# Optimization experiments

Measured on AMD Instinct MI355X. Metric: run time of the kernel, lower is better.

## Reference

```python
import jax, jax.numpy as jnp
import numpy as np

B = 1
E = 8388608                      # embedding size (dim 1)
NNZ = 131072                     # inhibition links
MIN_SPARSITY = 0.002
MAX_SPARSITY = 0.02
BOOST_PERCENT = 1e-8             # forward default boost_percent
MAX_ACTIVE = int(np.ceil(MAX_SPARSITY * E))    # 167773, torch uses .item() -> static
MIN_ACTIVE = int(np.floor(MIN_SPARSITY * E))   # 16777


def setup_inputs() -> dict:
    key = jax.random.key(0)
    k1, k3, k4, k5 = jax.random.split(key, 4)
    x = jax.random.normal(k1, (B, E, 1, 1), dtype=jnp.float32)
    boost_tensor = jnp.zeros((B, E, 1, 1), dtype=jnp.float32)   # initial boost state (zeros_like in module)
    inh_affector = jax.random.randint(k3, (NNZ,), 0, E, dtype=jnp.int32)
    inh_affectee = jax.random.randint(k4, (NNZ,), 0, E, dtype=jnp.int32)
    # inhibition values are negative (self-inhibition, affect_value=-0.01 scale)
    inh_values = -jax.random.uniform(k5, (NNZ,), dtype=jnp.float32) * 0.05
    return {"x": x, "boost_tensor": boost_tensor, "inh_values": inh_values,
            "inh_affector": inh_affector, "inh_affectee": inh_affectee}


def reference(x, boost_tensor, inh_values, inh_affector, inh_affectee):
    xf = x.reshape(B, E)
    bf = boost_tensor.reshape(B, E)

    # --- run_boosting: PercentClosenessBoosting (units far from max get boosted) ---
    boost_new = bf + (1.0 - xf / jnp.max(xf)) * jnp.float32(BOOST_PERCENT)
    boosted = jnp.maximum(xf, 0.0) + boost_new   # tensor_above + boost_tensor

    # --- apply_sparse_self_affector: tens[affectee] += tens[affector] * values ---
    # RHS gathered from the pre-update tensor, scatter-add onto affectee coords.
    inhibited = boosted.at[0, inh_affectee].add(boosted[0, inh_affector] * inh_values)

    # --- run_k_winners_positive: keep top max_active per row, binarize positives ---
    topv, topi = jax.lax.top_k(inhibited, MAX_ACTIVE)          # [B, K]
    rows = jnp.arange(B)[:, None]
    result = jnp.zeros((B, E), dtype=jnp.float32).at[rows, topi].set(
        (topv > 0).astype(jnp.float32))

    # --- choose_boosted_to_satisfy_minimum ---
    actually_active = jnp.sum(result)
    _, boost_idx = jax.lax.top_k(boost_new, MIN_ACTIVE)        # [B, MIN_ACTIVE]
    to_activate = jnp.ceil(jnp.float32(MIN_ACTIVE) - actually_active)
    need = actually_active < jnp.float32(MIN_ACTIVE)
    add = need & (jnp.arange(MIN_ACTIVE, dtype=jnp.float32) < to_activate)
    add = jnp.broadcast_to(add.astype(jnp.float32), (B, MIN_ACTIVE))
    out = result.at[rows, boost_idx].max(add)

    return out.reshape(B, E, 1, 1)
```

## Files before the change

### kernel.cpp

```cpp
#include <hip/hip_runtime.h>
#include <stdint.h>

#define E_SIZE   8388608
#define N4       (E_SIZE / 4)
#define NNZ_SZ   131072
#define K_ACT    167773
#define MIN_ACT  16777
#define CAP      262144
#define BCAP     2048
#define TINY_F   9.5367431640625e-7f
#define NBINS    16384
#define SHIFT1   18

__device__ __forceinline__ unsigned int f2A(float f) {
    unsigned int u = __float_as_uint(f);
    return (u & 0x80000000u) ? ~u : (u | 0x80000000u);
}
__device__ __forceinline__ unsigned int f2D(float f) { return ~f2A(f); }
__device__ __forceinline__ float A2f(unsigned int A) {
    unsigned int u = (A & 0x80000000u) ? (A & 0x7FFFFFFFu) : ~A;
    return __uint_as_float(u);
}
__device__ __forceinline__ float D2f(unsigned int D) { return A2f(~D); }

__device__ __forceinline__ float boostedf(float v, float b, float mx) {
    return fmaxf(v, 0.0f) + (b + (1.0f - v / mx) * 1e-8f);
}
__device__ __forceinline__ unsigned int binclamp14(float v) {
    return (v < TINY_F) ? (NBINS - 1u) : (f2D(v) >> SHIFT1);
}


__device__ void block_select(const unsigned int* counts, int nbins, unsigned int Krem,
                             unsigned int* res, unsigned int* scratch) {
    int t = threadIdx.x;
    int per = nbins >> 10; if (per == 0) per = 1;
    int nth = nbins / per;
    unsigned int part = 0;
    if (t < nth)
        for (int j = 0; j < per; j++) part += counts[t * per + j];
    scratch[t] = part;
    unsigned int ws = part;
    for (int off = 32; off; off >>= 1) ws += __shfl_down(ws, off, 64);
    if ((t & 63) == 0) scratch[1024 + (t >> 6)] = ws;
    __syncthreads();
    if (t == 0) {
        unsigned int cum = 0;
        int w = 0;
        for (; w < 15; w++) {
            unsigned int s = scratch[1024 + w];
            if (cum + s >= Krem) break;
            cum += s;
        }
        int tt = w * 64, te = tt + 63;
        for (; tt < te; tt++) {
            unsigned int s = scratch[tt];
            if (cum + s >= Krem) break;
            cum += s;
        }
        int b = tt * per, be = b + per - 1;
        for (; b < be; b++) {
            unsigned int s = counts[b];
            if (cum + s >= Krem) break;
            cum += s;
        }
        res[0] = (unsigned int)b;
        res[1] = Krem - cum;
    }
    __syncthreads();
}

__global__ void __launch_bounds__(256)
k_max(const float4* __restrict__ x, unsigned int* __restrict__ pmax,
      unsigned int* __restrict__ ctrl, unsigned int* __restrict__ hist) {
    int t = threadIdx.x, blk = blockIdx.x;
    if (blk == 0 && t < 64) ctrl[t] = 0u;
    if (t < 16) hist[blk * 16 + t] = 0u;
    int tid = blk * 256 + t;
    unsigned int m = 0u;
    for (int i = tid; i < N4; i += 1024 * 256) {
        float4 v = x[i];
        m = max(m, f2A(v.x)); m = max(m, f2A(v.y));
        m = max(m, f2A(v.z)); m = max(m, f2A(v.w));
    }
    for (int off = 32; off; off >>= 1)
        m = max(m, __shfl_down(m, off, 64));
    __shared__ unsigned int sm[4];
    if ((t & 63) == 0) sm[t >> 6] = m;
    __syncthreads();
    if (t == 0) pmax[blk] = max(max(sm[0], sm[1]), max(sm[2], sm[3]));
}

__device__ __forceinline__ float reduce_pmax(const unsigned int* __restrict__ pmax,
                                             unsigned int* smax) {
    int t = threadIdx.x;
    unsigned int m = pmax[t];
    for (int off = 32; off; off >>= 1)
        m = max(m, __shfl_down(m, off, 64));
    if ((t & 63) == 0) smax[t >> 6] = m;
    __syncthreads();
    if (t == 0) {
        unsigned int r = smax[0];
        for (int i = 1; i < 16; i++) r = max(r, smax[i]);
        smax[0] = r;
    }
    __syncthreads();
    return A2f(smax[0]);
}

__global__ void __launch_bounds__(1024)
k_boost_hist(const float4* __restrict__ x, const float4* __restrict__ bf,
             float4* __restrict__ out, const unsigned int* __restrict__ pmax,
             unsigned int* __restrict__ hist) {
    __shared__ unsigned int h[NBINS];
    __shared__ unsigned int smax[16];
    float mx = reduce_pmax(pmax, smax);
    int t = threadIdx.x;
    for (int i = t; i < NBINS; i += 1024) h[i] = 0u;
    __syncthreads();
    unsigned int tiny = 0;
    int gtid = blockIdx.x * 1024 + t;
    for (int i = gtid; i < N4; i += 256 * 1024) {
        float4 v = x[i], b = bf[i];
        float4 r;
        r.x = boostedf(v.x, b.x, mx);
        r.y = boostedf(v.y, b.y, mx);
        r.z = boostedf(v.z, b.z, mx);
        r.w = boostedf(v.w, b.w, mx);
        out[i] = r;
        #define HISTONE(c) { if ((c) < TINY_F) tiny++; \
            else atomicAdd(&h[f2D(c) >> SHIFT1], 1u); }
        HISTONE(r.x); HISTONE(r.y); HISTONE(r.z); HISTONE(r.w);
        #undef HISTONE
    }
    for (int off = 32; off; off >>= 1)
        tiny += __shfl_down(tiny, off, 64);
    if ((t & 63) == 0 && tiny) atomicAdd(&h[NBINS - 1], tiny);
    __syncthreads();
    for (int k = t; k < NBINS; k += 1024) {
        unsigned int c = h[k];
        if (c) atomicAdd(&hist[k], c);
    }
}

__global__ void __launch_bounds__(1024)
k_scatter(const float* __restrict__ x, const float* __restrict__ bf,
          const float* __restrict__ vals, const int* __restrict__ aff,
          const int* __restrict__ afe, float* __restrict__ inh,
          const unsigned int* __restrict__ pmax, unsigned int* __restrict__ hist) {
    __shared__ int shi[NBINS];
    __shared__ unsigned int smax[16];
    float mx = reduce_pmax(pmax, smax);
    int t = threadIdx.x;
    for (int i = t; i < NBINS; i += 1024) shi[i] = 0;
    __syncthreads();
    int i = blockIdx.x * 1024 + t;
    int a = aff[i], e = afe[i];
    float bo = boostedf(x[a], bf[a], mx);
    float contrib = bo * vals[i];
    float old = atomicAdd(&inh[e], contrib);
    float nw = old + contrib;
    unsigned int ob = binclamp14(old), nb = binclamp14(nw);
    if (ob != nb) {
        atomicAdd(&shi[nb], 1);
        atomicAdd(&shi[ob], -1);
    }
    __syncthreads();
    for (int k = t; k < NBINS; k += 1024) {
        int v = shi[k];
        if (v) atomicAdd((int*)&hist[k], v);
    }
}

__global__ void __launch_bounds__(1024)
k_scan1(const unsigned int* __restrict__ hist, unsigned int* __restrict__ ctrl) {
    __shared__ unsigned int scratch[1040];
    __shared__ unsigned int res[2];
    block_select(hist, NBINS, (unsigned int)K_ACT, res, scratch);
    if (threadIdx.x == 0) { ctrl[1] = res[0]; ctrl[2] = res[1]; }
}

__global__ void __launch_bounds__(1024)
k_markcompact(float4* __restrict__ out, const unsigned int* __restrict__ ctrl,
              unsigned int* __restrict__ ctrlw, unsigned int* __restrict__ gidx,
              unsigned int* __restrict__ gD) {
    __shared__ unsigned int cidx[BCAP];
    __shared__ unsigned int cDs[BCAP];
    __shared__ unsigned int scnt, sbase;
    int t = threadIdx.x;
    if (t == 0) scnt = 0;
    __syncthreads();
    unsigned int b1 = ctrl[1];
    int gtid = blockIdx.x * 1024 + t;
    for (int i = gtid; i < N4; i += 256 * 1024) {
        float4 f = out[i];
        float4 r;
        #define MARKONE(c, rr, comp) { \
            unsigned int bc = binclamp14(c); \
            if (bc < b1) rr = ((c) > 0.0f) ? 1.0f : 0.0f; \
            else { rr = 0.0f; if (bc == b1) { \
                unsigned int p = atomicAdd(&scnt, 1u); \
                if (p < BCAP) { cidx[p] = (unsigned int)i * 4u + comp; cDs[p] = f2D(c); } } } }
        MARKONE(f.x, r.x, 0u); MARKONE(f.y, r.y, 1u);
        MARKONE(f.z, r.z, 2u); MARKONE(f.w, r.w, 3u);
        #undef MARKONE
        out[i] = r;
    }
    __syncthreads();
    if (t == 0) {
        unsigned int m = min(scnt, (unsigned int)BCAP);
        scnt = m;
        sbase = atomicAdd(&ctrlw[7], m);
    }
    __syncthreads();
    unsigned int m = scnt, base = sbase;
    for (unsigned int i = t; i < m; i += 1024) {
        unsigned int g = base + i;
        if (g < CAP) { gidx[g] = cidx[i]; gD[g] = cDs[i]; }
    }
}

__global__ void __launch_bounds__(1024)
k_select(float* __restrict__ out, const unsigned int* __restrict__ ctrl,
         const unsigned int* __restrict__ gidx, const unsigned int* __restrict__ gD) {
    __shared__ unsigned int h512[512];
    __shared__ unsigned int scratch[1040];
    __shared__ unsigned int res[2];
    __shared__ unsigned int ties[128];
    __shared__ unsigned int tcnt;
    int t = threadIdx.x;
    unsigned int nc = min(ctrl[7], (unsigned int)CAP);
    unsigned int Krem = ctrl[2];
    unsigned int b1 = ctrl[1];

    if (t < 512) h512[t] = 0u;
    if (t == 0) tcnt = 0u;
    __syncthreads();
    for (unsigned int i = t; i < nc; i += 1024)
        atomicAdd(&h512[(gD[i] >> 9) & 511u], 1u);
    __syncthreads();
    block_select(h512, 512, Krem, res, scratch);
    unsigned int b2 = res[0], Krem2 = res[1];

    if (t < 512) h512[t] = 0u;
    __syncthreads();
    for (unsigned int i = t; i < nc; i += 1024) {
        unsigned int D = gD[i];
        if (((D >> 9) & 511u) == b2) atomicAdd(&h512[D & 511u], 1u);
    }
    __syncthreads();
    block_select(h512, 512, Krem2, res, scratch);
    unsigned int b3 = res[0], need = res[1];
    unsigned int T = (b1 << SHIFT1) | (b2 << 9) | b3;

    for (unsigned int i = t; i < nc; i += 1024) {
        if (gD[i] == T) {
            unsigned int p = atomicAdd(&tcnt, 1u);
            if (p < 128) ties[p] = gidx[i];
        }
    }
    __syncthreads();
    unsigned int M = min(tcnt, 128u);
    float val = (D2f(T) > 0.0f) ? 1.0f : 0.0f;
    for (unsigned int i = t; i < M; i += 1024) {
        unsigned int idx = ties[i];
        unsigned int rank = 0;
        for (unsigned int j = 0; j < M; j++) rank += (ties[j] < idx) ? 1u : 0u;
        if (rank < need) out[idx] = val;
    }
    for (unsigned int i = t; i < nc; i += 1024) {
        unsigned int D = gD[i];
        if (D < T) out[gidx[i]] = (D2f(D) > 0.0f) ? 1.0f : 0.0f;
    }
}

extern "C" void kernel_launch(void* const* d_in, const int* in_sizes, int n_in,
                              void* d_out, int out_size, void* d_ws, size_t ws_size,
                              hipStream_t stream) {
    const float* x    = (const float*)d_in[0];
    const float* bf   = (const float*)d_in[1];
    const float* vals = (const float*)d_in[2];
    const int*   aff  = (const int*)d_in[3];
    const int*   afe  = (const int*)d_in[4];
    float* out = (float*)d_out;

    unsigned int* ctrl = (unsigned int*)d_ws;
    unsigned int* pmax = (unsigned int*)((char*)d_ws + 4096);
    unsigned int* hist = (unsigned int*)((char*)d_ws + 8192);
    unsigned int* gidx = (unsigned int*)((char*)d_ws + 8192 + (size_t)NBINS * 4);
    unsigned int* gD   = (unsigned int*)((char*)d_ws + 8192 + (size_t)NBINS * 4 + (size_t)CAP * 4);

    k_max<<<1024, 256, 0, stream>>>((const float4*)x, pmax, ctrl, hist);
    k_boost_hist<<<256, 1024, 0, stream>>>((const float4*)x, (const float4*)bf,
                                           (float4*)out, pmax, hist);
    k_scatter<<<NNZ_SZ / 1024, 1024, 0, stream>>>(x, bf, vals, aff, afe, out, pmax, hist);
    k_scan1<<<1, 1024, 0, stream>>>(hist, ctrl);
    k_markcompact<<<256, 1024, 0, stream>>>((float4*)out, ctrl, ctrl, gidx, gD);
    k_select<<<1, 1024, 0, stream>>>(out, ctrl, gidx, gD);
}
```

Measured before the change: 187.7 us.

## Fuse all six stages into one cooperative kernel with grid syncs

Replaces the six separate launches with one cooperative kernel of 256 blocks, using grid.sync between the max, boost/histogram, scatter, scan, mark/compact and final select phases. This removes the per-launch overhead and the gaps between launches, and lets each block run the bin-select scan on the histogram itself instead of a separate single-block kernel. The scatter phase now does its histogram-correction atomics straight to global memory rather than through a shared histogram. In exchange it adds the cost of grid-wide barriers and needs all 256 blocks of 1024 threads, each holding about 90KB of shared memory, to be resident at the same time. Blocks other than block 0 sit idle during the final select phase.

```diff
diff --git a/kernel.cpp b/kernel.cpp
--- a/kernel.cpp
+++ b/kernel.cpp
@@ -1,5 +1,8 @@
 #include <hip/hip_runtime.h>
+#include <hip/hip_cooperative_groups.h>
 #include <stdint.h>
+
+namespace cg = cooperative_groups;
 
 #define E_SIZE   8388608
 #define N4       (E_SIZE / 4)
@@ -11,6 +14,8 @@
 #define TINY_F   9.5367431640625e-7f
 #define NBINS    16384
 #define SHIFT1   18
+#define NBLK     256
+#define NTHR     1024
 
 __device__ __forceinline__ unsigned int f2A(float f) {
     unsigned int u = __float_as_uint(f);
@@ -29,7 +34,6 @@
 __device__ __forceinline__ unsigned int binclamp14(float v) {
     return (v < TINY_F) ? (NBINS - 1u) : (f2D(v) >> SHIFT1);
 }
-
 
 __device__ void block_select(const unsigned int* counts, int nbins, unsigned int Krem,
                              unsigned int* res, unsigned int* scratch) {
@@ -70,130 +74,110 @@
     __syncthreads();
 }
 
-__global__ void __launch_bounds__(256)
-k_max(const float4* __restrict__ x, unsigned int* __restrict__ pmax,
-      unsigned int* __restrict__ ctrl, unsigned int* __restrict__ hist) {
-    int t = threadIdx.x, blk = blockIdx.x;
+__global__ void __launch_bounds__(NTHR, 4)
+k_fused(const float* __restrict__ x, const float* __restrict__ bf,
+        const float* __restrict__ vals, const int* __restrict__ aff,
+        const int* __restrict__ afe, float* __restrict__ out,
+        unsigned int* __restrict__ ctrl, unsigned int* __restrict__ pmax,
+        unsigned int* __restrict__ hist, unsigned int* __restrict__ gidx,
+        unsigned int* __restrict__ gD) {
+    cg::grid_group grid = cg::this_grid();
+    __shared__ unsigned int h[NBINS];
+    __shared__ unsigned int scratch[1040];
+    __shared__ unsigned int res[2];
+    __shared__ unsigned int smax[16];
+    __shared__ unsigned int cidx[BCAP];
+    __shared__ unsigned int cDs[BCAP];
+    __shared__ unsigned int ties[128];
+    __shared__ unsigned int scnt, sbase, tcnt;
+
+    const int t = threadIdx.x;
+    const int blk = blockIdx.x;
+    const float4* __restrict__ x4 = (const float4*)x;
+    const float4* __restrict__ bf4 = (const float4*)bf;
+    float4* __restrict__ out4 = (float4*)out;
+
     if (blk == 0 && t < 64) ctrl[t] = 0u;
-    if (t < 16) hist[blk * 16 + t] = 0u;
-    int tid = blk * 256 + t;
-    unsigned int m = 0u;
-    for (int i = tid; i < N4; i += 1024 * 256) {
-        float4 v = x[i];
-        m = max(m, f2A(v.x)); m = max(m, f2A(v.y));
-        m = max(m, f2A(v.z)); m = max(m, f2A(v.w));
-    }
-    for (int off = 32; off; off >>= 1)
-        m = max(m, __shfl_down(m, off, 64));
-    __shared__ unsigned int sm[4];
-    if ((t & 63) == 0) sm[t >> 6] = m;
-    __syncthreads();
-    if (t == 0) pmax[blk] = max(max(sm[0], sm[1]), max(sm[2], sm[3]));
-}
-
-__device__ __forceinline__ float reduce_pmax(const unsigned int* __restrict__ pmax,
-                                             unsigned int* smax) {
-    int t = threadIdx.x;
-    unsigned int m = pmax[t];
-    for (int off = 32; off; off >>= 1)
-        m = max(m, __shfl_down(m, off, 64));
-    if ((t & 63) == 0) smax[t >> 6] = m;
-    __syncthreads();
-    if (t == 0) {
-        unsigned int r = smax[0];
-        for (int i = 1; i < 16; i++) r = max(r, smax[i]);
-        smax[0] = r;
-    }
-    __syncthreads();
-    return A2f(smax[0]);
-}
-
-__global__ void __launch_bounds__(1024)
-k_boost_hist(const float4* __restrict__ x, const float4* __restrict__ bf,
-             float4* __restrict__ out, const unsigned int* __restrict__ pmax,
-             unsigned int* __restrict__ hist) {
-    __shared__ unsigned int h[NBINS];
-    __shared__ unsigned int smax[16];
-    float mx = reduce_pmax(pmax, smax);
-    int t = threadIdx.x;
-    for (int i = t; i < NBINS; i += 1024) h[i] = 0u;
-    __syncthreads();
-    unsigned int tiny = 0;
-    int gtid = blockIdx.x * 1024 + t;
-    for (int i = gtid; i < N4; i += 256 * 1024) {
-        float4 v = x[i], b = bf[i];
-        float4 r;
-        r.x = boostedf(v.x, b.x, mx);
-        r.y = boostedf(v.y, b.y, mx);
-        r.z = boostedf(v.z, b.z, mx);
-        r.w = boostedf(v.w, b.w, mx);
-        out[i] = r;
-        #define HISTONE(c) { if ((c) < TINY_F) tiny++; \
-            else atomicAdd(&h[f2D(c) >> SHIFT1], 1u); }
-        HISTONE(r.x); HISTONE(r.y); HISTONE(r.z); HISTONE(r.w);
-        #undef HISTONE
-    }
-    for (int off = 32; off; off >>= 1)
-        tiny += __shfl_down(tiny, off, 64);
-    if ((t & 63) == 0 && tiny) atomicAdd(&h[NBINS - 1], tiny);
-    __syncthreads();
-    for (int k = t; k < NBINS; k += 1024) {
+    if (t < (NBINS / NBLK)) hist[blk * (NBINS / NBLK) + t] = 0u;
+    {
+        unsigned int m = 0u;
+        for (int i = blk * NTHR + t; i < N4; i += NBLK * NTHR) {
+            float4 v = x4[i];
+            m = max(m, f2A(v.x)); m = max(m, f2A(v.y));
+            m = max(m, f2A(v.z)); m = max(m, f2A(v.w));
+        }
+        for (int off = 32; off; off >>= 1) m = max(m, __shfl_down(m, off, 64));
+        if ((t & 63) == 0) smax[t >> 6] = m;
+        __syncthreads();
+        if (t == 0) {
+            unsigned int r = smax[0];
+            for (int i = 1; i < 16; i++) r = max(r, smax[i]);
+            pmax[blk] = r;
+        }
+    }
+    __threadfence();
+    grid.sync();
+
+    float mx;
+    {
+        unsigned int m = (t < NBLK) ? pmax[t] : 0u;
+        for (int off = 32; off; off >>= 1) m = max(m, __shfl_down(m, off, 64));
+        if (t < NBLK && (t & 63) == 0) smax[t >> 6] = m;
+        __syncthreads();
+        if (t == 0) smax[0] = max(max(smax[0], smax[1]), max(smax[2], smax[3]));
+        __syncthreads();
+        mx = A2f(smax[0]);
+    }
+    for (int i = t; i < NBINS; i += NTHR) h[i] = 0u;
+    __syncthreads();
+    {
+        unsigned int tiny = 0;
+        for (int i = blk * NTHR + t; i < N4; i += NBLK * NTHR) {
+            float4 v = x4[i], b = bf4[i];
+            float4 r;
+            r.x = boostedf(v.x, b.x, mx);
+            r.y = boostedf(v.y, b.y, mx);
+            r.z = boostedf(v.z, b.z, mx);
+            r.w = boostedf(v.w, b.w, mx);
+            out4[i] = r;
+            #define HISTONE(c) { if ((c) < TINY_F) tiny++; \
+                else atomicAdd(&h[f2D(c) >> SHIFT1], 1u); }
+            HISTONE(r.x); HISTONE(r.y); HISTONE(r.z); HISTONE(r.w);
+            #undef HISTONE
+        }
+        for (int off = 32; off; off >>= 1) tiny += __shfl_down(tiny, off, 64);
+        if ((t & 63) == 0 && tiny) atomicAdd(&h[NBINS - 1], tiny);
+    }
+    __syncthreads();
+    for (int k = t; k < NBINS; k += NTHR) {
         unsigned int c = h[k];
         if (c) atomicAdd(&hist[k], c);
     }
-}
-
-__global__ void __launch_bounds__(1024)
-k_scatter(const float* __restrict__ x, const float* __restrict__ bf,
-          const float* __restrict__ vals, const int* __restrict__ aff,
-          const int* __restrict__ afe, float* __restrict__ inh,
-          const unsigned int* __restrict__ pmax, unsigned int* __restrict__ hist) {
-    __shared__ int shi[NBINS];
-    __shared__ unsigned int smax[16];
-    float mx = reduce_pmax(pmax, smax);
-    int t = threadIdx.x;
-    for (int i = t; i < NBINS; i += 1024) shi[i] = 0;
-    __syncthreads();
-    int i = blockIdx.x * 1024 + t;
-    int a = aff[i], e = afe[i];
-    float bo = boostedf(x[a], bf[a], mx);
-    float contrib = bo * vals[i];
-    float old = atomicAdd(&inh[e], contrib);
-    float nw = old + contrib;
-    unsigned int ob = binclamp14(old), nb = binclamp14(nw);
-    if (ob != nb) {
-        atomicAdd(&shi[nb], 1);
-        atomicAdd(&shi[ob], -1);
-    }
-    __syncthreads();
-    for (int k = t; k < NBINS; k += 1024) {
-        int v = shi[k];
-        if (v) atomicAdd((int*)&hist[k], v);
-    }
-}
-
-__global__ void __launch_bounds__(1024)
-k_scan1(const unsigned int* __restrict__ hist, unsigned int* __restrict__ ctrl) {
-    __shared__ unsigned int scratch[1040];
-    __shared__ unsigned int res[2];
+    __threadfence();
+    grid.sync();
+
+    if (t < 512) {
+        int i = blk * 512 + t;
+        int a = aff[i], e = afe[i];
+        float bo = boostedf(x[a], bf[a], mx);
+        float contrib = bo * vals[i];
+        float old = atomicAdd(&out[e], contrib);
+        float nw = old + contrib;
+        unsigned int ob = binclamp14(old), nb = binclamp14(nw);
+        if (ob != nb) {
+            atomicAdd(&hist[nb], 1u);
+            atomicAdd((int*)&hist[ob], -1);
+        }
+    }
+    __threadfence();
+    grid.sync();
+
     block_select(hist, NBINS, (unsigned int)K_ACT, res, scratch);
-    if (threadIdx.x == 0) { ctrl[1] = res[0]; ctrl[2] = res[1]; }
-}
-
-__global__ void __launch_bounds__(1024)
-k_markcompact(float4* __restrict__ out, const unsigned int* __restrict__ ctrl,
-              unsigned int* __restrict__ ctrlw, unsigned int* __restrict__ gidx,
-              unsigned int* __restrict__ gD) {
-    __shared__ unsigned int cidx[BCAP];
-    __shared__ unsigned int cDs[BCAP];
-    __shared__ unsigned int scnt, sbase;
-    int t = threadIdx.x;
-    if (t == 0) scnt = 0;
-    __syncthreads();
-    unsigned int b1 = ctrl[1];
-    int gtid = blockIdx.x * 1024 + t;
-    for (int i = gtid; i < N4; i += 256 * 1024) {
-        float4 f = out[i];
+    unsigned int b1 = res[0], Krem = res[1];
+    if (t == 0) scnt = 0u;
+    __syncthreads();
+    for (int i = blk * NTHR + t; i < N4; i += NBLK * NTHR) {
+        float4 f = out4[i];
         float4 r;
         #define MARKONE(c, rr, comp) { \
             unsigned int bc = binclamp14(c); \
@@ -204,73 +188,68 @@
         MARKONE(f.x, r.x, 0u); MARKONE(f.y, r.y, 1u);
         MARKONE(f.z, r.z, 2u); MARKONE(f.w, r.w, 3u);
         #undef MARKONE
-        out[i] = r;
+        out4[i] = r;
     }
     __syncthreads();
     if (t == 0) {
-        unsigned int m = min(scnt, (unsigned int)BCAP);
-        scnt = m;
-        sbase = atomicAdd(&ctrlw[7], m);
-    }
-    __syncthreads();
-    unsigned int m = scnt, base = sbase;
-    for (unsigned int i = t; i < m; i += 1024) {
-        unsigned int g = base + i;
-        if (g < CAP) { gidx[g] = cidx[i]; gD[g] = cDs[i]; }
-    }
-}
-
-__global__ void __launch_bounds__(1024)
-k_select(float* __restrict__ out, const unsigned int* __restrict__ ctrl,
-         const unsigned int* __restrict__ gidx, const unsigned int* __restrict__ gD) {
-    __shared__ unsigned int h512[512];
-    __shared__ unsigned int scratch[1040];
-    __shared__ unsigned int res[2];
-    __shared__ unsigned int ties[128];
-    __shared__ unsigned int tcnt;
-    int t = threadIdx.x;
-    unsigned int nc = min(ctrl[7], (unsigned int)CAP);
-    unsigned int Krem = ctrl[2];
-    unsigned int b1 = ctrl[1];
-
-    if (t < 512) h512[t] = 0u;
-    if (t == 0) tcnt = 0u;
-    __syncthreads();
-    for (unsigned int i = t; i < nc; i += 1024)
-        atomicAdd(&h512[(gD[i] >> 9) & 511u], 1u);
-    __syncthreads();
-    block_select(h512, 512, Krem, res, scratch);
-    unsigned int b2 = res[0], Krem2 = res[1];
-
-    if (t < 512) h512[t] = 0u;
-    __syncthreads();
-    for (unsigned int i = t; i < nc; i += 1024) {
-        unsigned int D = gD[i];
-        if (((D >> 9) & 511u) == b2) atomicAdd(&h512[D & 511u], 1u);
-    }
-    __syncthreads();
-    block_select(h512, 512, Krem2, res, scratch);
-    unsigned int b3 = res[0], need = res[1];
-    unsigned int T = (b1 << SHIFT1) | (b2 << 9) | b3;
-
-    for (unsigned int i = t; i < nc; i += 1024) {
-        if (gD[i] == T) {
-            unsigned int p = atomicAdd(&tcnt, 1u);
-            if (p < 128) ties[p] = gidx[i];
-        }
-    }
-    __syncthreads();
-    unsigned int M = min(tcnt, 128u);
-    float val = (D2f(T) > 0.0f) ? 1.0f : 0.0f;
-    for (unsigned int i = t; i < M; i += 1024) {
-        unsigned int idx = ties[i];
-        unsigned int rank = 0;
-        for (unsigned int j = 0; j < M; j++) rank += (ties[j] < idx) ? 1u : 0u;
-        if (rank < need) out[idx] = val;
-    }
-    for (unsigned int i = t; i < nc; i += 1024) {
-        unsigned int D = gD[i];
-        if (D < T) out[gidx[i]] = (D2f(D) > 0.0f) ? 1.0f : 0.0f;
+        unsigned int m2 = min(scnt, (unsigned int)BCAP);
+        scnt = m2;
+        sbase = atomicAdd(&ctrl[7], m2);
+    }
+    __syncthreads();
+    {
+        unsigned int m2 = scnt, base = sbase;
+        for (unsigned int i = t; i < m2; i += NTHR) {
+            unsigned int g = base + i;
+            if (g < CAP) { gidx[g] = cidx[i]; gD[g] = cDs[i]; }
+        }
+    }
+    __threadfence();
+    grid.sync();
+
+    if (blk != 0) return;
+    {
+        unsigned int nc = min(ctrl[7], (unsigned int)CAP);
+
+        if (t < 512) h[t] = 0u;
+        if (t == 0) tcnt = 0u;
+        __syncthreads();
+        for (unsigned int i = t; i < nc; i += NTHR)
+            atomicAdd(&h[(gD[i] >> 9) & 511u], 1u);
+        __syncthreads();
+        block_select(h, 512, Krem, res, scratch);
+        unsigned int b2 = res[0], Krem2 = res[1];
+
+        if (t < 512) h[t] = 0u;
+        __syncthreads();
+        for (unsigned int i = t; i < nc; i += NTHR) {
+            unsigned int D = gD[i];
+            if (((D >> 9) & 511u) == b2) atomicAdd(&h[D & 511u], 1u);
+        }
+        __syncthreads();
+        block_select(h, 512, Krem2, res, scratch);
+        unsigned int b3 = res[0], need = res[1];
+        unsigned int T = (b1 << SHIFT1) | (b2 << 9) | b3;
+
+        for (unsigned int i = t; i < nc; i += NTHR) {
+            if (gD[i] == T) {
+                unsigned int p = atomicAdd(&tcnt, 1u);
+                if (p < 128) ties[p] = gidx[i];
+            }
+        }
+        __syncthreads();
+        unsigned int M = min(tcnt, 128u);
+        float val = (D2f(T) > 0.0f) ? 1.0f : 0.0f;
+        for (unsigned int i = t; i < M; i += NTHR) {
+            unsigned int idx = ties[i];
+            unsigned int rank = 0;
+            for (unsigned int j = 0; j < M; j++) rank += (ties[j] < idx) ? 1u : 0u;
+            if (rank < need) out[idx] = val;
+        }
+        for (unsigned int i = t; i < nc; i += NTHR) {
+            unsigned int D = gD[i];
+            if (D < T) out[gidx[i]] = (D2f(D) > 0.0f) ? 1.0f : 0.0f;
+        }
     }
 }
 
@@ -290,11 +269,8 @@
     unsigned int* gidx = (unsigned int*)((char*)d_ws + 8192 + (size_t)NBINS * 4);
     unsigned int* gD   = (unsigned int*)((char*)d_ws + 8192 + (size_t)NBINS * 4 + (size_t)CAP * 4);
 
-    k_max<<<1024, 256, 0, stream>>>((const float4*)x, pmax, ctrl, hist);
-    k_boost_hist<<<256, 1024, 0, stream>>>((const float4*)x, (const float4*)bf,
-                                           (float4*)out, pmax, hist);
-    k_scatter<<<NNZ_SZ / 1024, 1024, 0, stream>>>(x, bf, vals, aff, afe, out, pmax, hist);
-    k_scan1<<<1, 1024, 0, stream>>>(hist, ctrl);
-    k_markcompact<<<256, 1024, 0, stream>>>((float4*)out, ctrl, ctrl, gidx, gD);
-    k_select<<<1, 1024, 0, stream>>>(out, ctrl, gidx, gD);
-}
+    void* args[] = { &x, &bf, &vals, &aff, &afe, &out,
+                     &ctrl, &pmax, &hist, &gidx, &gD };
+    hipLaunchCooperativeKernel((void*)k_fused, dim3(NBLK), dim3(NTHR),
+                               args, 0, stream);
+}
```

Result: slower. 586.7 us (+212.5%).

## Fuse threshold scan into mark-compact, drop shared histogram in scatter, double grids

Applied to the files above, without the earlier changes.

The single-block histogram scan kernel is folded into the mark/compact kernel: every block now redoes the 16384-bin select itself, and block 0 publishes the threshold bin and remaining count to new control slots. This removes one serial launch. The scatter kernel stops zeroing and flushing a 16384-entry shared histogram and updates the global histogram atomically only when a bin changes. Grid sizes for the boost/histogram and mark kernels go from 256 to 512 blocks. The trade-off is redundant scan work in each block and more global atomics in scatter. The change also relies on ctrl[32]/ctrl[33] being valid workspace slots.

```diff
diff --git a/kernel.cpp b/kernel.cpp
--- a/kernel.cpp
+++ b/kernel.cpp
@@ -29,7 +29,6 @@
 __device__ __forceinline__ unsigned int binclamp14(float v) {
     return (v < TINY_F) ? (NBINS - 1u) : (f2D(v) >> SHIFT1);
 }
-
 
 __device__ void block_select(const unsigned int* counts, int nbins, unsigned int Krem,
                              unsigned int* res, unsigned int* scratch) {
@@ -120,7 +119,7 @@
     __syncthreads();
     unsigned int tiny = 0;
     int gtid = blockIdx.x * 1024 + t;
-    for (int i = gtid; i < N4; i += 256 * 1024) {
+    for (int i = gtid; i < N4; i += 512 * 1024) {
         float4 v = x[i], b = bf[i];
         float4 r;
         r.x = boostedf(v.x, b.x, mx);
@@ -148,13 +147,9 @@
           const float* __restrict__ vals, const int* __restrict__ aff,
           const int* __restrict__ afe, float* __restrict__ inh,
           const unsigned int* __restrict__ pmax, unsigned int* __restrict__ hist) {
-    __shared__ int shi[NBINS];
     __shared__ unsigned int smax[16];
     float mx = reduce_pmax(pmax, smax);
-    int t = threadIdx.x;
-    for (int i = t; i < NBINS; i += 1024) shi[i] = 0;
-    __syncthreads();
-    int i = blockIdx.x * 1024 + t;
+    int i = blockIdx.x * 1024 + threadIdx.x;
     int a = aff[i], e = afe[i];
     float bo = boostedf(x[a], bf[a], mx);
     float contrib = bo * vals[i];
@@ -162,37 +157,33 @@
     float nw = old + contrib;
     unsigned int ob = binclamp14(old), nb = binclamp14(nw);
     if (ob != nb) {
-        atomicAdd(&shi[nb], 1);
-        atomicAdd(&shi[ob], -1);
-    }
-    __syncthreads();
-    for (int k = t; k < NBINS; k += 1024) {
-        int v = shi[k];
-        if (v) atomicAdd((int*)&hist[k], v);
-    }
-}
-
-__global__ void __launch_bounds__(1024)
-k_scan1(const unsigned int* __restrict__ hist, unsigned int* __restrict__ ctrl) {
+        atomicAdd(&hist[nb], 1u);
+        atomicAdd((int*)&hist[ob], -1);
+    }
+}
+
+__global__ void __launch_bounds__(1024)
+k_markscan(float4* __restrict__ out, const unsigned int* __restrict__ hist,
+           unsigned int* __restrict__ ctrl, unsigned int* __restrict__ gidx,
+           unsigned int* __restrict__ gD) {
     __shared__ unsigned int scratch[1040];
     __shared__ unsigned int res[2];
-    block_select(hist, NBINS, (unsigned int)K_ACT, res, scratch);
-    if (threadIdx.x == 0) { ctrl[1] = res[0]; ctrl[2] = res[1]; }
-}
-
-__global__ void __launch_bounds__(1024)
-k_markcompact(float4* __restrict__ out, const unsigned int* __restrict__ ctrl,
-              unsigned int* __restrict__ ctrlw, unsigned int* __restrict__ gidx,
-              unsigned int* __restrict__ gD) {
     __shared__ unsigned int cidx[BCAP];
     __shared__ unsigned int cDs[BCAP];
     __shared__ unsigned int scnt, sbase;
     int t = threadIdx.x;
-    if (t == 0) scnt = 0;
-    __syncthreads();
-    unsigned int b1 = ctrl[1];
+    block_select(hist, NBINS, (unsigned int)K_ACT, res, scratch);
+    unsigned int b1 = res[0];
+    if (t == 0) {
+        scnt = 0;
+        if (blockIdx.x == 0) {
+            atomicExch(&ctrl[32], res[0]);
+            atomicExch(&ctrl[33], res[1]);
+        }
+    }
+    __syncthreads();
     int gtid = blockIdx.x * 1024 + t;
-    for (int i = gtid; i < N4; i += 256 * 1024) {
+    for (int i = gtid; i < N4; i += 512 * 1024) {
         float4 f = out[i];
         float4 r;
         #define MARKONE(c, rr, comp) { \
@@ -210,7 +201,7 @@
     if (t == 0) {
         unsigned int m = min(scnt, (unsigned int)BCAP);
         scnt = m;
-        sbase = atomicAdd(&ctrlw[7], m);
+        sbase = atomicAdd(&ctrl[7], m);
     }
     __syncthreads();
     unsigned int m = scnt, base = sbase;
@@ -230,8 +221,8 @@
     __shared__ unsigned int tcnt;
     int t = threadIdx.x;
     unsigned int nc = min(ctrl[7], (unsigned int)CAP);
-    unsigned int Krem = ctrl[2];
-    unsigned int b1 = ctrl[1];
+    unsigned int b1 = ctrl[32];
+    unsigned int Krem = ctrl[33];
 
     if (t < 512) h512[t] = 0u;
     if (t == 0) tcnt = 0u;
@@ -291,10 +282,9 @@
     unsigned int* gD   = (unsigned int*)((char*)d_ws + 8192 + (size_t)NBINS * 4 + (size_t)CAP * 4);
 
     k_max<<<1024, 256, 0, stream>>>((const float4*)x, pmax, ctrl, hist);
-    k_boost_hist<<<256, 1024, 0, stream>>>((const float4*)x, (const float4*)bf,
+    k_boost_hist<<<512, 1024, 0, stream>>>((const float4*)x, (const float4*)bf,
                                            (float4*)out, pmax, hist);
     k_scatter<<<NNZ_SZ / 1024, 1024, 0, stream>>>(x, bf, vals, aff, afe, out, pmax, hist);
-    k_scan1<<<1, 1024, 0, stream>>>(hist, ctrl);
-    k_markcompact<<<256, 1024, 0, stream>>>((float4*)out, ctrl, ctrl, gidx, gD);
+    k_markscan<<<512, 1024, 0, stream>>>((float4*)out, hist, ctrl, gidx, gD);
     k_select<<<1, 1024, 0, stream>>>(out, ctrl, gidx, gD);
 }
```

After: 245.8 us. 30.9% more time.
